# Optimization experiments

Measured on AMD Instinct MI355X. Metric: run time of the kernel, lower is better.

Reference implementation:

```python
import jax, jax.numpy as jnp
import numpy as np

B, S, H = 4, 1024, 896
NH, HD = 16, 56          # num_heads, head_dim (NH*HD == H)
SD = 896                 # ssm_state_dim
EPS = 1e-5


def _ln(v, g, b):
    m = jnp.mean(v, axis=-1, keepdims=True)
    var = jnp.var(v, axis=-1, keepdims=True)
    return (v - m) * jax.lax.rsqrt(var + EPS) * g + b


def setup_inputs() -> dict:
    key = jax.random.key(0)
    ks = jax.random.split(key, 24)
    n = lambda k, sh, s=0.02: jax.random.normal(k, sh, dtype=jnp.float32) * s
    return {
        "x": jax.random.normal(ks[0], (B, S, H), dtype=jnp.float32),
        # SSM params
        "A": n(ks[1], (SD, SD), 0.05),
        "Bm": n(ks[2], (SD, H), 0.05),
        "Cm": n(ks[3], (H, SD), 0.05),
        "ssm_in_w": n(ks[4], (H, H)), "ssm_in_b": n(ks[5], (H,)),
        "ssm_out_w": n(ks[6], (H, H)), "ssm_out_b": n(ks[7], (H,)),
        # MHA params (torch in_proj packs q,k,v)
        "qkv_w": n(ks[8], (3 * H, H)), "qkv_b": n(ks[9], (3 * H,)),
        "attn_out_w": n(ks[10], (H, H)), "attn_out_b": n(ks[11], (H,)),
        "proj_w": n(ks[12], (H, H)), "proj_b": n(ks[13], (H,)),
        # LayerNorms
        "ln_ssm_g": jnp.ones((H,), jnp.float32), "ln_ssm_b": jnp.zeros((H,), jnp.float32),
        "ln_attn_g": jnp.ones((H,), jnp.float32), "ln_attn_b": jnp.zeros((H,), jnp.float32),
        # Mixer
        "fuse_w": n(ks[14], (H, 3 * H)), "fuse_b": n(ks[15], (H,)),
        "gate_w": n(ks[16], (2, H)), "gate_b": n(ks[17], (2,)),
    }


def reference(x, A, Bm, Cm, ssm_in_w, ssm_in_b, ssm_out_w, ssm_out_b,
              qkv_w, qkv_b, attn_out_w, attn_out_b, proj_w, proj_b,
              ln_ssm_g, ln_ssm_b, ln_attn_g, ln_attn_b,
              fuse_w, fuse_b, gate_w, gate_b):
    # ---- SSM head: h_t = tanh(h_{t-1} A^T + x_t B^T); y_t = h_t C^T ----
    xp = x @ ssm_in_w.T + ssm_in_b                     # (B,S,H)
    xB = xp @ Bm.T                                     # precompute input drive (B,S,SD)

    def step(h, xb_t):
        h = jnp.tanh(h @ A.T + xb_t)
        return h, h

    h0 = jnp.zeros((B, SD), x.dtype)
    _, hs = jax.lax.scan(step, h0, jnp.swapaxes(xB, 0, 1))   # hs: (S,B,SD)
    ys = jnp.swapaxes(hs, 0, 1) @ Cm.T                 # (B,S,H)
    ssm_out = ys @ ssm_out_w.T + ssm_out_b

    # ---- Attention head: standard non-causal MHA + extra projection ----
    qkv = x @ qkv_w.T + qkv_b                          # (B,S,3H)
    q, k, v = jnp.split(qkv, 3, axis=-1)
    q = q.reshape(B, S, NH, HD)
    k = k.reshape(B, S, NH, HD)
    v = v.reshape(B, S, NH, HD)
    scores = jnp.einsum("bqhd,bkhd->bhqk", q, k) / np.sqrt(HD).astype(np.float32)
    attn = jax.nn.softmax(scores, axis=-1)
    ctx = jnp.einsum("bhqk,bkhd->bqhd", attn, v).reshape(B, S, H)
    attn_out = (ctx @ attn_out_w.T + attn_out_b) @ proj_w.T + proj_b

    # ---- Gate norms ----
    ssm_g = _ln(ssm_out, ln_ssm_g, ln_ssm_b)
    attn_g = _ln(attn_out, ln_attn_g, ln_attn_b)

    # ---- Mixing network (memory_state=None -> zero padding) ----
    combined = jnp.concatenate([ssm_g, attn_g, jnp.zeros_like(ssm_g)], axis=-1)
    fused = combined @ fuse_w.T + fuse_b
    gates = jax.nn.softmax(fused @ gate_w.T + gate_b, axis=-1)   # (B,S,2)
    out = gates[..., 0:1] * ssm_g + gates[..., 1:2] * attn_g
    return out  # dropout is identity in eval mode
```

## Files before the change

kernel.cpp:

```cpp
#include <hip/hip_runtime.h>
#include <hip/hip_bf16.h>

typedef __bf16 bf16;
typedef __bf16 bf16x8 __attribute__((ext_vector_type(8)));
typedef __bf16 bf16x4 __attribute__((ext_vector_type(4)));
typedef float  f32x4  __attribute__((ext_vector_type(4)));

__global__ __launch_bounds__(256, 2)
void gemm128_kernel(const float* __restrict__ A, const float* __restrict__ B,
                    const float* __restrict__ bias, float* __restrict__ C,
                    int M, int N, int K, int lda, int ldb, int ldc)
{
    __shared__ bf16 As[128][72];
    __shared__ bf16 Bs[128][72];
    const int tid = threadIdx.x;
    const long bm = (long)blockIdx.y * 128;
    const long bn = (long)blockIdx.x * 128;
    const int w  = tid >> 6;
    const int l  = tid & 63;
    const int wm = (w >> 1) * 64, wn = (w & 1) * 64;
    const int lr = l & 15, lk = (l >> 4) * 8;

    const int srow = tid >> 1;
    const int scol = (tid & 1) * 32;
    const float* Ap = A + (bm + srow) * (long)lda + scol;
    const float* Bp = B + (bn + srow) * (long)ldb + scol;

    f32x4 acc[4][4];
    #pragma unroll
    for (int i = 0; i < 4; ++i)
        #pragma unroll
        for (int j = 0; j < 4; ++j)
            acc[i][j] = f32x4{0.f, 0.f, 0.f, 0.f};

    for (int kt = 0; kt < K; kt += 64) {
        #pragma unroll
        for (int i = 0; i < 32; i += 4) {
            float4 av = *reinterpret_cast<const float4*>(Ap + kt + i);
            float4 bv = *reinterpret_cast<const float4*>(Bp + kt + i);
            bf16x4 ac; ac[0] = (bf16)av.x; ac[1] = (bf16)av.y; ac[2] = (bf16)av.z; ac[3] = (bf16)av.w;
            bf16x4 bc; bc[0] = (bf16)bv.x; bc[1] = (bf16)bv.y; bc[2] = (bf16)bv.z; bc[3] = (bf16)bv.w;
            *reinterpret_cast<bf16x4*>(&As[srow][scol + i]) = ac;
            *reinterpret_cast<bf16x4*>(&Bs[srow][scol + i]) = bc;
        }
        __syncthreads();
        #pragma unroll
        for (int kk = 0; kk < 64; kk += 32) {
            bf16x8 a[4], b[4];
            #pragma unroll
            for (int i = 0; i < 4; ++i) {
                a[i] = *reinterpret_cast<const bf16x8*>(&As[wm + i * 16 + lr][kk + lk]);
                b[i] = *reinterpret_cast<const bf16x8*>(&Bs[wn + i * 16 + lr][kk + lk]);
            }
            #pragma unroll
            for (int i = 0; i < 4; ++i)
                #pragma unroll
                for (int j = 0; j < 4; ++j)
                    acc[i][j] = __builtin_amdgcn_mfma_f32_16x16x32_bf16(a[i], b[j], acc[i][j], 0, 0, 0);
        }
        __syncthreads();
    }
    const int crow = wm + (l >> 4) * 4;
    const int ccol = wn + (l & 15);
    #pragma unroll
    for (int i = 0; i < 4; ++i)
        #pragma unroll
        for (int j = 0; j < 4; ++j) {
            long col = bn + ccol + j * 16;
            float bv = bias ? bias[col] : 0.0f;
            #pragma unroll
            for (int r = 0; r < 4; ++r) {
                long row = bm + crow + i * 16 + r;
                C[row * (long)ldc + col] = acc[i][j][r] + bv;
            }
        }
}

#define SENT64 0xFFFFFFFFFFFFFFFFull
#define NBLK_SCAN 56

__device__ __forceinline__ float lo32f(unsigned long long v) {
    return __builtin_bit_cast(float, (unsigned int)v);
}
__device__ __forceinline__ float hi32f(unsigned long long v) {
    return __builtin_bit_cast(float, (unsigned int)(v >> 32));
}

__device__ __forceinline__ void scan_body(const float* __restrict__ Amat,
                                          const float* __restrict__ xB,
                                          float* __restrict__ hs,
                                          unsigned long long* __restrict__ Y,
                                          float* hS)
{
    __builtin_amdgcn_s_setprio(3);
    const int tid = threadIdx.x;
    const int bi  = blockIdx.x;
    const int kq  = tid & 31;
    const int rg  = tid >> 5;
    const int row = bi * 16 + rg;

    float4 areg[7];
    {
        const float4* Ap = reinterpret_cast<const float4*>(Amat + (long)row * 896 + kq * 28);
        #pragma unroll
        for (int j = 0; j < 7; ++j) areg[j] = Ap[j];
    }

    const int d0 = tid;
    const int d1 = tid + 512;
    const bool two = (tid < 384);

    for (int t = 1; t <= 1024; ++t) {
        const long so = (long)(t - 1) * 896 + row;
        float xb0 = 0, xb1 = 0, xb2 = 0, xb3 = 0;
        if (kq == 0) {
            xb0 = xB[so];
            xb1 = xB[so +  917504];
            xb2 = xB[so + 1835008];
            xb3 = xB[so + 2752512];
        }

        if (t == 1) {
            #pragma unroll
            for (int j = 0; j < 7; ++j) hS[tid + j * 512] = 0.0f;
        } else {
            const unsigned long long* Yp = Y + (long)(t - 2) * 1792;
            unsigned long long va, vb, vc = 0, vd = 0;
            for (;;) {
                va = __hip_atomic_load(&Yp[2 * d0],     __ATOMIC_RELAXED, __HIP_MEMORY_SCOPE_AGENT);
                vb = __hip_atomic_load(&Yp[2 * d0 + 1], __ATOMIC_RELAXED, __HIP_MEMORY_SCOPE_AGENT);
                bool ok = (va != SENT64) & (vb != SENT64);
                if (two) {
                    vc = __hip_atomic_load(&Yp[2 * d1],     __ATOMIC_RELAXED, __HIP_MEMORY_SCOPE_AGENT);
                    vd = __hip_atomic_load(&Yp[2 * d1 + 1], __ATOMIC_RELAXED, __HIP_MEMORY_SCOPE_AGENT);
                    ok &= (vc != SENT64) & (vd != SENT64);
                }
                if (ok) break;
                __builtin_amdgcn_s_sleep(1);
            }
            hS[       d0] = lo32f(va);
            hS[ 896 + d0] = hi32f(va);
            hS[1792 + d0] = lo32f(vb);
            hS[2688 + d0] = hi32f(vb);
            if (two) {
                hS[       d1] = lo32f(vc);
                hS[ 896 + d1] = hi32f(vc);
                hS[1792 + d1] = lo32f(vd);
                hS[2688 + d1] = hi32f(vd);
            }
        }
        __syncthreads();

        const float4* h0p = reinterpret_cast<const float4*>(hS +    0 + kq * 28);
        const float4* h1p = reinterpret_cast<const float4*>(hS +  896 + kq * 28);
        const float4* h2p = reinterpret_cast<const float4*>(hS + 1792 + kq * 28);
        const float4* h3p = reinterpret_cast<const float4*>(hS + 2688 + kq * 28);
        float a0 = 0, a1 = 0, a2 = 0, a3 = 0;
        #pragma unroll
        for (int j = 0; j < 7; ++j) {
            float4 a = areg[j];
            float4 v0 = h0p[j]; a0 += a.x*v0.x + a.y*v0.y + a.z*v0.z + a.w*v0.w;
            float4 v1 = h1p[j]; a1 += a.x*v1.x + a.y*v1.y + a.z*v1.z + a.w*v1.w;
            float4 v2 = h2p[j]; a2 += a.x*v2.x + a.y*v2.y + a.z*v2.z + a.w*v2.w;
            float4 v3 = h3p[j]; a3 += a.x*v3.x + a.y*v3.y + a.z*v3.z + a.w*v3.w;
        }
        a0 += __shfl_xor(a0, 16); a1 += __shfl_xor(a1, 16); a2 += __shfl_xor(a2, 16); a3 += __shfl_xor(a3, 16);
        a0 += __shfl_xor(a0,  8); a1 += __shfl_xor(a1,  8); a2 += __shfl_xor(a2,  8); a3 += __shfl_xor(a3,  8);
        a0 += __shfl_xor(a0,  4); a1 += __shfl_xor(a1,  4); a2 += __shfl_xor(a2,  4); a3 += __shfl_xor(a3,  4);
        a0 += __shfl_xor(a0,  2); a1 += __shfl_xor(a1,  2); a2 += __shfl_xor(a2,  2); a3 += __shfl_xor(a3,  2);
        a0 += __shfl_xor(a0,  1); a1 += __shfl_xor(a1,  1); a2 += __shfl_xor(a2,  1); a3 += __shfl_xor(a3,  1);

        if (kq == 0) {
            float z[4] = { a0 + xb0, a1 + xb1, a2 + xb2, a3 + xb3 };
            float hv[4];
            #pragma unroll
            for (int b = 0; b < 4; ++b) {
                float zz = fminf(fmaxf(z[b], -15.f), 15.f);
                float e  = __expf(2.f * zz);
                hv[b] = (e - 1.f) / (e + 1.f);
            }
            unsigned long long lo =
                (unsigned long long)__builtin_bit_cast(unsigned int, hv[0]) |
                ((unsigned long long)__builtin_bit_cast(unsigned int, hv[1]) << 32);
            unsigned long long hi =
                (unsigned long long)__builtin_bit_cast(unsigned int, hv[2]) |
                ((unsigned long long)__builtin_bit_cast(unsigned int, hv[3]) << 32);
            unsigned long long* yp = Y + (long)(t - 1) * 1792 + 2 * row;
            __hip_atomic_store(&yp[0], lo, __ATOMIC_RELAXED, __HIP_MEMORY_SCOPE_AGENT);
            __hip_atomic_store(&yp[1], hi, __ATOMIC_RELAXED, __HIP_MEMORY_SCOPE_AGENT);
            #pragma unroll
            for (int b = 0; b < 4; ++b)
                hs[(long)b * 917504 + so] = hv[b];
        }
        __syncthreads();
    }
}

__device__ __forceinline__ void attn_body(const float* __restrict__ qkv,
                                          float* __restrict__ ctx,
                                          float* ldsf, int bid2)
{
    float* qS = ldsf;
    float* pS = qS + 1792;
    float* rS = pS + 2112;
    float* lS = rS + 32;
    bf16*  kS = (bf16*)(lS + 32);
    bf16*  vS = kS + 3840;

    const int tid = threadIdx.x;
    const int qc = bid2 & 31;
    const int h  = (bid2 >> 5) & 15;
    const int b  = bid2 >> 9;
    const long base = (long)b * 1024 * 2688;
    const int q0 = qc * 32;
    const int hoff = h * 56;

    for (int idx = tid; idx < 1792; idx += 512) {
        int r = idx / 56, d = idx - r * 56;
        qS[idx] = qkv[base + (long)(q0 + r) * 2688 + hoff + d] * 0.13363062095621f;
    }

    const int w = tid >> 6, l = tid & 63;
    const int qrow = 4 * w;
    const int oq = tid >> 4, ods = tid & 15;
    float m0 = -3e38f, m1 = -3e38f, m2 = -3e38f, m3 = -3e38f;
    float s_l0 = 0, s_l1 = 0, s_l2 = 0, s_l3 = 0;
    float o0 = 0, o1 = 0, o2 = 0, o3 = 0;

    for (int kt = 0; kt < 16; ++kt) {
        __syncthreads();
        for (int idx = tid; idx < 3584; idx += 512) {
            int r = idx / 56, d = idx - r * 56;
            long g = base + (long)(kt * 64 + r) * 2688 + hoff + d;
            kS[r * 60 + d] = (bf16)qkv[g + 896];
            vS[r * 60 + d] = (bf16)qkv[g + 1792];
        }
        __syncthreads();

        float s0 = 0, s1 = 0, s2 = 0, s3 = 0;
        const float* qp = qS + qrow * 56;
        const bf16* kp = kS + l * 60;
        #pragma unroll 8
        for (int d = 0; d < 56; ++d) {
            float kv = (float)kp[d];
            s0 += qp[d] * kv; s1 += qp[d + 56] * kv;
            s2 += qp[d + 112] * kv; s3 += qp[d + 168] * kv;
        }
        float x0 = s0, x1 = s1, x2 = s2, x3 = s3;
        #pragma unroll
        for (int off = 32; off >= 1; off >>= 1) {
            x0 = fmaxf(x0, __shfl_xor(x0, off));
            x1 = fmaxf(x1, __shfl_xor(x1, off));
            x2 = fmaxf(x2, __shfl_xor(x2, off));
            x3 = fmaxf(x3, __shfl_xor(x3, off));
        }
        float nm0 = fmaxf(m0, x0), nm1 = fmaxf(m1, x1);
        float nm2 = fmaxf(m2, x2), nm3 = fmaxf(m3, x3);
        float p0 = __expf(s0 - nm0), p1 = __expf(s1 - nm1);
        float p2 = __expf(s2 - nm2), p3 = __expf(s3 - nm3);
        float sc0 = __expf(m0 - nm0), sc1 = __expf(m1 - nm1);
        float sc2 = __expf(m2 - nm2), sc3 = __expf(m3 - nm3);
        float t0 = p0, t1 = p1, t2 = p2, t3 = p3;
        #pragma unroll
        for (int off = 32; off >= 1; off >>= 1) {
            t0 += __shfl_xor(t0, off); t1 += __shfl_xor(t1, off);
            t2 += __shfl_xor(t2, off); t3 += __shfl_xor(t3, off);
        }
        s_l0 = s_l0 * sc0 + t0; s_l1 = s_l1 * sc1 + t1;
        s_l2 = s_l2 * sc2 + t2; s_l3 = s_l3 * sc3 + t3;
        m0 = nm0; m1 = nm1; m2 = nm2; m3 = nm3;
        pS[(qrow + 0) * 66 + l] = p0; pS[(qrow + 1) * 66 + l] = p1;
        pS[(qrow + 2) * 66 + l] = p2; pS[(qrow + 3) * 66 + l] = p3;
        if (l == 0) { rS[qrow] = sc0; rS[qrow+1] = sc1; rS[qrow+2] = sc2; rS[qrow+3] = sc3; }
        __syncthreads();

        float rf = rS[oq];
        o0 *= rf; o1 *= rf; o2 *= rf; o3 *= rf;
        const float* pp = pS + oq * 66;
        #pragma unroll 4
        for (int kk = 0; kk < 64; ++kk) {
            float p = pp[kk];
            const bf16* vp = vS + kk * 60 + ods;
            o0 += p * (float)vp[0];
            o1 += p * (float)vp[16];
            o2 += p * (float)vp[32];
            if (ods < 8) o3 += p * (float)vp[48];
        }
    }
    __syncthreads();
    if (l == 0) {
        lS[qrow]     = 1.f / s_l0; lS[qrow + 1] = 1.f / s_l1;
        lS[qrow + 2] = 1.f / s_l2; lS[qrow + 3] = 1.f / s_l3;
    }
    __syncthreads();
    float inv = lS[oq];
    float* cp = ctx + ((long)b * 1024 + q0 + oq) * 896 + hoff + ods;
    cp[0]  = o0 * inv;
    cp[16] = o1 * inv;
    cp[32] = o2 * inv;
    if (ods < 8) cp[48] = o3 * inv;
}

__global__ __launch_bounds__(512)
void scan_attn_kernel(const float* __restrict__ Amat, const float* __restrict__ xB,
                      float* __restrict__ hs, unsigned long long* __restrict__ Y,
                      const float* __restrict__ qkv, float* __restrict__ ctx)
{
    __shared__ float ldsf[7872];
    if (blockIdx.x < NBLK_SCAN)
        scan_body(Amat, xB, hs, Y, ldsf);
    else
        attn_body(qkv, ctx, ldsf, blockIdx.x - NBLK_SCAN);
}

__global__ __launch_bounds__(256)
void ln2_kernel(const float* __restrict__ s_in, const float* __restrict__ a_in,
                const float* __restrict__ gs, const float* __restrict__ bs,
                const float* __restrict__ ga, const float* __restrict__ ba,
                float* __restrict__ comb)
{
    const int wv = threadIdx.x >> 6, ln = threadIdx.x & 63;
    const long row = (long)blockIdx.x * 4 + wv;
    const bool is_a = (blockIdx.y != 0);
    const float* src = (is_a ? a_in : s_in) + row * 896;
    float v[14]; float sum = 0, sq = 0;
    #pragma unroll
    for (int j = 0; j < 14; ++j) { v[j] = src[ln + j * 64]; sum += v[j]; sq += v[j] * v[j]; }
    #pragma unroll
    for (int off = 32; off >= 1; off >>= 1) { sum += __shfl_xor(sum, off); sq += __shfl_xor(sq, off); }
    const float mean = sum * (1.0f / 896.0f);
    const float var  = sq * (1.0f / 896.0f) - mean * mean;
    const float inv  = rsqrtf(var + 1e-5f);
    const float* g  = is_a ? ga : gs;
    const float* bb = is_a ? ba : bs;
    float* dst = comb + row * 1792 + (is_a ? 896 : 0);
    #pragma unroll
    for (int j = 0; j < 14; ++j) {
        int i = ln + j * 64;
        dst[i] = (v[j] - mean) * inv * g[i] + bb[i];
    }
}

__global__ __launch_bounds__(256)
void gate_mix_kernel(const float* __restrict__ fused, const float* __restrict__ gw,
                     const float* __restrict__ gb, const float* __restrict__ comb,
                     float* __restrict__ out)
{
    const int tid = threadIdx.x;
    const int seg = tid & 15;
    const long row = (long)blockIdx.x * 16 + (tid >> 4);
    const float* fr = fused + row * 896;
    float d0 = 0, d1 = 0;
    for (int i = seg; i < 896; i += 16) {
        float f = fr[i];
        d0 += f * gw[i];
        d1 += f * gw[896 + i];
    }
    #pragma unroll
    for (int off = 8; off >= 1; off >>= 1) { d0 += __shfl_xor(d0, off); d1 += __shfl_xor(d1, off); }
    float l0 = d0 + gb[0], l1 = d1 + gb[1];
    float m = fmaxf(l0, l1);
    float e0 = __expf(l0 - m), e1 = __expf(l1 - m);
    float inv = 1.0f / (e0 + e1);
    float g0 = e0 * inv, g1 = e1 * inv;
    const float* cr = comb + row * 1792;
    float* orow = out + row * 896;
    for (int i = seg; i < 896; i += 16)
        orow[i] = g0 * cr[i] + g1 * cr[896 + i];
}

extern "C" void kernel_launch(void* const* d_in, const int* in_sizes, int n_in,
                              void* d_out, int out_size, void* d_ws, size_t ws_size,
                              hipStream_t stream)
{
    (void)in_sizes; (void)n_in; (void)out_size; (void)ws_size;
    const float* x         = (const float*)d_in[0];
    const float* Amat      = (const float*)d_in[1];
    const float* Bm        = (const float*)d_in[2];
    const float* Cm        = (const float*)d_in[3];
    const float* ssm_in_w  = (const float*)d_in[4];
    const float* ssm_in_b  = (const float*)d_in[5];
    const float* ssm_out_w = (const float*)d_in[6];
    const float* ssm_out_b = (const float*)d_in[7];
    const float* qkv_w     = (const float*)d_in[8];
    const float* qkv_b     = (const float*)d_in[9];
    const float* attn_w    = (const float*)d_in[10];
    const float* attn_b    = (const float*)d_in[11];
    const float* proj_w    = (const float*)d_in[12];
    const float* proj_b    = (const float*)d_in[13];
    const float* ln_sg     = (const float*)d_in[14];
    const float* ln_sb     = (const float*)d_in[15];
    const float* ln_ag     = (const float*)d_in[16];
    const float* ln_ab     = (const float*)d_in[17];
    const float* fuse_w    = (const float*)d_in[18];
    const float* fuse_b    = (const float*)d_in[19];
    const float* gate_w    = (const float*)d_in[20];
    const float* gate_b    = (const float*)d_in[21];

    float* ws = (float*)d_ws;
    const long S0 = 0;
    const long S1 = 3670016;
    const long S2 = 7340032;
    const long S3 = 18350080;
    const long S4 = 22020096;
    const long S5 = 25690112;
    const long S6 = 33030144;

    dim3 g128(7, 32), gqkv(21, 32);

    gemm128_kernel<<<g128, 256, 0, stream>>>(x, ssm_in_w, ssm_in_b, ws + S0, 4096, 896, 896, 896, 896, 896);
    gemm128_kernel<<<g128, 256, 0, stream>>>(ws + S0, Bm, nullptr, ws + S1, 4096, 896, 896, 896, 896, 896);
    hipMemsetAsync(ws + S0, 0xFF, 3670016 * sizeof(float), stream);
    gemm128_kernel<<<gqkv, 256, 0, stream>>>(x, qkv_w, qkv_b, ws + S2, 4096, 2688, 896, 896, 896, 2688);
    scan_attn_kernel<<<NBLK_SCAN + 2048, 512, 0, stream>>>(
        Amat, ws + S1, ws + S3, (unsigned long long*)(ws + S0), ws + S2, ws + S6);
    gemm128_kernel<<<g128, 256, 0, stream>>>(ws + S3, Cm, nullptr, ws + S0, 4096, 896, 896, 896, 896, 896);
    gemm128_kernel<<<g128, 256, 0, stream>>>(ws + S0, ssm_out_w, ssm_out_b, ws + S4, 4096, 896, 896, 896, 896, 896);
    gemm128_kernel<<<g128, 256, 0, stream>>>(ws + S6, attn_w, attn_b, ws + S1, 4096, 896, 896, 896, 896, 896);
    gemm128_kernel<<<g128, 256, 0, stream>>>(ws + S1, proj_w, proj_b, ws + S3, 4096, 896, 896, 896, 896, 896);
    ln2_kernel<<<dim3(1024, 2), 256, 0, stream>>>(ws + S4, ws + S3, ln_sg, ln_sb, ln_ag, ln_ab, ws + S5);
    gemm128_kernel<<<g128, 256, 0, stream>>>(ws + S5, fuse_w, fuse_b, ws + S4, 4096, 896, 1792, 1792, 2688, 896);
    gate_mix_kernel<<<256, 256, 0, stream>>>(ws + S4, gate_w, gate_b, ws + S5, (float*)d_out);
}
```

Baseline: 3.225 ms.

## Convert operands to bf16 upfront and stream GEMM tiles via global_load_lds

Adds a batched fp32-to-bf16 conversion kernel for x and the weights. The GEMM now takes bf16 operands and loads tiles straight into LDS with global_load_lds instead of converting in registers. Intermediate activations (hs, ctx, xp, ys, comb) are written as bf16 so the following GEMMs read half the bytes, and the scan's barriers become a bare s_barrier after an lgkmcnt wait. In exchange it adds conversion launches, drops the LDS row padding (which may cause bank conflicts), and takes on a more complex workspace aliasing plan.

```diff
diff --git a/kernel.cpp b/kernel.cpp
--- a/kernel.cpp
+++ b/kernel.cpp
@@ -6,25 +6,54 @@
 typedef __bf16 bf16x4 __attribute__((ext_vector_type(4)));
 typedef float  f32x4  __attribute__((ext_vector_type(4)));
 
+#define AS1 __attribute__((address_space(1)))
+#define AS3 __attribute__((address_space(3)))
+
+struct CvtArgs {
+    const float* src[5];
+    bf16* dst[5];
+    int rows[5], cols[5], src_ld[5];
+};
+
+__global__ __launch_bounds__(256)
+void cvt_kernel(CvtArgs a)
+{
+    const int t = blockIdx.y;
+    const float* s = a.src[t];
+    bf16* d = a.dst[t];
+    const int cols = a.cols[t];
+    const long total = (long)a.rows[t] * cols;
+    const int ld = a.src_ld[t];
+    for (long i = ((long)blockIdx.x * 256 + threadIdx.x) * 4; i < total;
+         i += (long)gridDim.x * 1024) {
+        long r = i / cols, c = i - r * cols;
+        float4 v = *reinterpret_cast<const float4*>(s + r * ld + c);
+        bf16x4 o; o[0] = (bf16)v.x; o[1] = (bf16)v.y; o[2] = (bf16)v.z; o[3] = (bf16)v.w;
+        *reinterpret_cast<bf16x4*>(d + i) = o;
+    }
+}
+
 __global__ __launch_bounds__(256, 2)
-void gemm128_kernel(const float* __restrict__ A, const float* __restrict__ B,
-                    const float* __restrict__ bias, float* __restrict__ C,
-                    int M, int N, int K, int lda, int ldb, int ldc)
-{
-    __shared__ bf16 As[128][72];
-    __shared__ bf16 Bs[128][72];
+void gemm_bf16_kernel(const bf16* __restrict__ A, const bf16* __restrict__ B,
+                      const float* __restrict__ bias,
+                      float* __restrict__ Cf, bf16* __restrict__ Cb,
+                      int M, int N, int K)
+{
+    __shared__ bf16 As[128 * 64];
+    __shared__ bf16 Bs[128 * 64];
     const int tid = threadIdx.x;
     const long bm = (long)blockIdx.y * 128;
     const long bn = (long)blockIdx.x * 128;
-    const int w  = tid >> 6;
-    const int l  = tid & 63;
+    const int w  = tid >> 6, l = tid & 63;
     const int wm = (w >> 1) * 64, wn = (w & 1) * 64;
     const int lr = l & 15, lk = (l >> 4) * 8;
 
-    const int srow = tid >> 1;
-    const int scol = (tid & 1) * 32;
-    const float* Ap = A + (bm + srow) * (long)lda + scol;
-    const float* Bp = B + (bn + srow) * (long)ldb + scol;
+    const int srow = tid >> 3;
+    const int scol = (tid & 7) * 8;
+    const bf16* Ag = A + (bm + srow) * (long)K + scol;
+    const bf16* Bg = B + (bn + srow) * (long)K + scol;
+    bf16* AsW = As + srow * 64 + scol;
+    bf16* BsW = Bs + srow * 64 + scol;
 
     f32x4 acc[4][4];
     #pragma unroll
@@ -35,13 +64,13 @@
 
     for (int kt = 0; kt < K; kt += 64) {
         #pragma unroll
-        for (int i = 0; i < 32; i += 4) {
-            float4 av = *reinterpret_cast<const float4*>(Ap + kt + i);
-            float4 bv = *reinterpret_cast<const float4*>(Bp + kt + i);
-            bf16x4 ac; ac[0] = (bf16)av.x; ac[1] = (bf16)av.y; ac[2] = (bf16)av.z; ac[3] = (bf16)av.w;
-            bf16x4 bc; bc[0] = (bf16)bv.x; bc[1] = (bf16)bv.y; bc[2] = (bf16)bv.z; bc[3] = (bf16)bv.w;
-            *reinterpret_cast<bf16x4*>(&As[srow][scol + i]) = ac;
-            *reinterpret_cast<bf16x4*>(&Bs[srow][scol + i]) = bc;
+        for (int i = 0; i < 4; ++i) {
+            __builtin_amdgcn_global_load_lds(
+                (const AS1 void*)(Ag + (long)i * 32 * K + kt),
+                (AS3 void*)(AsW + i * 2048), 16, 0, 0);
+            __builtin_amdgcn_global_load_lds(
+                (const AS1 void*)(Bg + (long)i * 32 * K + kt),
+                (AS3 void*)(BsW + i * 2048), 16, 0, 0);
         }
         __syncthreads();
         #pragma unroll
@@ -49,8 +78,8 @@
             bf16x8 a[4], b[4];
             #pragma unroll
             for (int i = 0; i < 4; ++i) {
-                a[i] = *reinterpret_cast<const bf16x8*>(&As[wm + i * 16 + lr][kk + lk]);
-                b[i] = *reinterpret_cast<const bf16x8*>(&Bs[wn + i * 16 + lr][kk + lk]);
+                a[i] = *reinterpret_cast<const bf16x8*>(&As[(wm + i * 16 + lr) * 64 + kk + lk]);
+                b[i] = *reinterpret_cast<const bf16x8*>(&Bs[(wn + i * 16 + lr) * 64 + kk + lk]);
             }
             #pragma unroll
             for (int i = 0; i < 4; ++i)
@@ -71,7 +100,9 @@
             #pragma unroll
             for (int r = 0; r < 4; ++r) {
                 long row = bm + crow + i * 16 + r;
-                C[row * (long)ldc + col] = acc[i][j][r] + bv;
+                float v = acc[i][j][r] + bv;
+                if (Cf) Cf[row * (long)N + col] = v;
+                if (Cb) Cb[row * (long)N + col] = (bf16)v;
             }
         }
 }
@@ -79,6 +110,11 @@
 #define SENT64 0xFFFFFFFFFFFFFFFFull
 #define NBLK_SCAN 56
 
+__device__ __forceinline__ void bar_lgkm() {
+    asm volatile("s_waitcnt lgkmcnt(0)" ::: "memory");
+    __builtin_amdgcn_s_barrier();
+}
+
 __device__ __forceinline__ float lo32f(unsigned long long v) {
     return __builtin_bit_cast(float, (unsigned int)v);
 }
@@ -88,7 +124,7 @@
 
 __device__ __forceinline__ void scan_body(const float* __restrict__ Amat,
                                           const float* __restrict__ xB,
-                                          float* __restrict__ hs,
+                                          bf16* __restrict__ hs16,
                                           unsigned long long* __restrict__ Y,
                                           float* hS)
 {
@@ -149,7 +185,7 @@
                 hS[2688 + d1] = hi32f(vd);
             }
         }
-        __syncthreads();
+        bar_lgkm();
 
         const float4* h0p = reinterpret_cast<const float4*>(hS +    0 + kq * 28);
         const float4* h1p = reinterpret_cast<const float4*>(hS +  896 + kq * 28);
@@ -190,14 +226,14 @@
             __hip_atomic_store(&yp[1], hi, __ATOMIC_RELAXED, __HIP_MEMORY_SCOPE_AGENT);
             #pragma unroll
             for (int b = 0; b < 4; ++b)
-                hs[(long)b * 917504 + so] = hv[b];
-        }
-        __syncthreads();
+                hs16[(long)b * 917504 + so] = (bf16)hv[b];
+        }
+        bar_lgkm();
     }
 }
 
 __device__ __forceinline__ void attn_body(const float* __restrict__ qkv,
-                                          float* __restrict__ ctx,
+                                          bf16* __restrict__ ctx16,
                                           float* ldsf, int bid2)
 {
     float* qS = ldsf;
@@ -294,30 +330,30 @@
     }
     __syncthreads();
     float inv = lS[oq];
-    float* cp = ctx + ((long)b * 1024 + q0 + oq) * 896 + hoff + ods;
-    cp[0]  = o0 * inv;
-    cp[16] = o1 * inv;
-    cp[32] = o2 * inv;
-    if (ods < 8) cp[48] = o3 * inv;
+    bf16* cp = ctx16 + ((long)b * 1024 + q0 + oq) * 896 + hoff + ods;
+    cp[0]  = (bf16)(o0 * inv);
+    cp[16] = (bf16)(o1 * inv);
+    cp[32] = (bf16)(o2 * inv);
+    if (ods < 8) cp[48] = (bf16)(o3 * inv);
 }
 
 __global__ __launch_bounds__(512)
 void scan_attn_kernel(const float* __restrict__ Amat, const float* __restrict__ xB,
-                      float* __restrict__ hs, unsigned long long* __restrict__ Y,
-                      const float* __restrict__ qkv, float* __restrict__ ctx)
+                      bf16* __restrict__ hs16, unsigned long long* __restrict__ Y,
+                      const float* __restrict__ qkv, bf16* __restrict__ ctx16)
 {
     __shared__ float ldsf[7872];
     if (blockIdx.x < NBLK_SCAN)
-        scan_body(Amat, xB, hs, Y, ldsf);
+        scan_body(Amat, xB, hs16, Y, ldsf);
     else
-        attn_body(qkv, ctx, ldsf, blockIdx.x - NBLK_SCAN);
+        attn_body(qkv, ctx16, ldsf, blockIdx.x - NBLK_SCAN);
 }
 
 __global__ __launch_bounds__(256)
 void ln2_kernel(const float* __restrict__ s_in, const float* __restrict__ a_in,
                 const float* __restrict__ gs, const float* __restrict__ bs,
                 const float* __restrict__ ga, const float* __restrict__ ba,
-                float* __restrict__ comb)
+                float* __restrict__ comb, bf16* __restrict__ comb16)
 {
     const int wv = threadIdx.x >> 6, ln = threadIdx.x & 63;
     const long row = (long)blockIdx.x * 4 + wv;
@@ -333,11 +369,14 @@
     const float inv  = rsqrtf(var + 1e-5f);
     const float* g  = is_a ? ga : gs;
     const float* bb = is_a ? ba : bs;
-    float* dst = comb + row * 1792 + (is_a ? 896 : 0);
+    float* dst   = comb   + row * 1792 + (is_a ? 896 : 0);
+    bf16*  dst16 = comb16 + row * 1792 + (is_a ? 896 : 0);
     #pragma unroll
     for (int j = 0; j < 14; ++j) {
         int i = ln + j * 64;
-        dst[i] = (v[j] - mean) * inv * g[i] + bb[i];
+        float o = (v[j] - mean) * inv * g[i] + bb[i];
+        dst[i] = o;
+        dst16[i] = (bf16)o;
     }
 }
 
@@ -397,28 +436,59 @@
     const float* gate_w    = (const float*)d_in[20];
     const float* gate_b    = (const float*)d_in[21];
 
-    float* ws = (float*)d_ws;
-    const long S0 = 0;
-    const long S1 = 3670016;
-    const long S2 = 7340032;
-    const long S3 = 18350080;
-    const long S4 = 22020096;
-    const long S5 = 25690112;
-    const long S6 = 33030144;
-
-    dim3 g128(7, 32), gqkv(21, 32);
-
-    gemm128_kernel<<<g128, 256, 0, stream>>>(x, ssm_in_w, ssm_in_b, ws + S0, 4096, 896, 896, 896, 896, 896);
-    gemm128_kernel<<<g128, 256, 0, stream>>>(ws + S0, Bm, nullptr, ws + S1, 4096, 896, 896, 896, 896, 896);
-    hipMemsetAsync(ws + S0, 0xFF, 3670016 * sizeof(float), stream);
-    gemm128_kernel<<<gqkv, 256, 0, stream>>>(x, qkv_w, qkv_b, ws + S2, 4096, 2688, 896, 896, 896, 2688);
-    scan_attn_kernel<<<NBLK_SCAN + 2048, 512, 0, stream>>>(
-        Amat, ws + S1, ws + S3, (unsigned long long*)(ws + S0), ws + S2, ws + S6);
-    gemm128_kernel<<<g128, 256, 0, stream>>>(ws + S3, Cm, nullptr, ws + S0, 4096, 896, 896, 896, 896, 896);
-    gemm128_kernel<<<g128, 256, 0, stream>>>(ws + S0, ssm_out_w, ssm_out_b, ws + S4, 4096, 896, 896, 896, 896, 896);
-    gemm128_kernel<<<g128, 256, 0, stream>>>(ws + S6, attn_w, attn_b, ws + S1, 4096, 896, 896, 896, 896, 896);
-    gemm128_kernel<<<g128, 256, 0, stream>>>(ws + S1, proj_w, proj_b, ws + S3, 4096, 896, 896, 896, 896, 896);
-    ln2_kernel<<<dim3(1024, 2), 256, 0, stream>>>(ws + S4, ws + S3, ln_sg, ln_sb, ln_ag, ln_ab, ws + S5);
-    gemm128_kernel<<<g128, 256, 0, stream>>>(ws + S5, fuse_w, fuse_b, ws + S4, 4096, 896, 1792, 1792, 2688, 896);
-    gate_mix_kernel<<<256, 256, 0, stream>>>(ws + S4, gate_w, gate_b, ws + S5, (float*)d_out);
-}
+    float* wsf = (float*)d_ws;
+    char*  wsb = (char*)d_ws;
+
+    unsigned long long* Y = (unsigned long long*)wsb;
+    float* xB       = wsf + 3670016;
+    float* qkv      = wsf + 7340032;
+    float* attn_out = wsf + 18350080;
+    float* ssm_out  = wsf + 22020096;
+    float* combf    = wsf + 25690112;
+    bf16* comb16 = (bf16*)wsb;
+    bf16* ssm_in_w16 = (bf16*)(wsb + 73400320);
+    bf16* Bm16       = (bf16*)(wsb + 75005952);
+    bf16* qkv_w16    = (bf16*)(wsb + 76611584);
+    bf16* hs16   = (bf16*)(wsb + 73400320);
+    bf16* ys16   = (bf16*)(wsb + 80740352);
+    bf16* Cm16        = (bf16*)(wsb + 14680064);
+    bf16* ssm_out_w16 = (bf16*)(wsb + 16285696);
+    bf16* attn_w16    = (bf16*)(wsb + 17891328);
+    bf16* proj_w16    = (bf16*)(wsb + 19496960);
+    bf16* fuse_w16    = (bf16*)(wsb + 21102592);
+    bf16* ctx16  = (bf16*)(wsb + 102760448);
+    bf16* t116   = (bf16*)(wsb + 110100480);
+    bf16* x16    = (bf16*)(wsb + 132120576);
+    bf16* xp16   = (bf16*)(wsb + 139460608);
+
+    hipMemsetAsync(Y, 0xFF, 14680064, stream);
+
+    CvtArgs c1{};
+    c1.src[0] = x;        c1.dst[0] = x16;        c1.rows[0] = 1;    c1.cols[0] = 3670016; c1.src_ld[0] = 3670016;
+    c1.src[1] = ssm_in_w; c1.dst[1] = ssm_in_w16; c1.rows[1] = 1;    c1.cols[1] = 802816;  c1.src_ld[1] = 802816;
+    c1.src[2] = Bm;       c1.dst[2] = Bm16;       c1.rows[2] = 1;    c1.cols[2] = 802816;  c1.src_ld[2] = 802816;
+    c1.src[3] = qkv_w;    c1.dst[3] = qkv_w16;    c1.rows[3] = 1;    c1.cols[3] = 2408448; c1.src_ld[3] = 2408448;
+    c1.src[4] = x;        c1.dst[4] = x16;        c1.rows[4] = 1;    c1.cols[4] = 0;       c1.src_ld[4] = 4;
+    cvt_kernel<<<dim3(64, 4), 256, 0, stream>>>(c1);
+
+    gemm_bf16_kernel<<<dim3(7, 32),  256, 0, stream>>>(x16,  ssm_in_w16, ssm_in_b, nullptr, xp16, 4096, 896, 896);
+    gemm_bf16_kernel<<<dim3(7, 32),  256, 0, stream>>>(xp16, Bm16,       nullptr,  xB, nullptr,  4096, 896, 896);
+    gemm_bf16_kernel<<<dim3(21, 32), 256, 0, stream>>>(x16,  qkv_w16,    qkv_b,    qkv, nullptr, 4096, 2688, 896);
+    scan_attn_kernel<<<NBLK_SCAN + 2048, 512, 0, stream>>>(Amat, xB, hs16, Y, qkv, ctx16);
+
+    CvtArgs c2{};
+    c2.src[0] = Cm;        c2.dst[0] = Cm16;        c2.rows[0] = 1;   c2.cols[0] = 802816; c2.src_ld[0] = 802816;
+    c2.src[1] = ssm_out_w; c2.dst[1] = ssm_out_w16; c2.rows[1] = 1;   c2.cols[1] = 802816; c2.src_ld[1] = 802816;
+    c2.src[2] = attn_w;    c2.dst[2] = attn_w16;    c2.rows[2] = 1;   c2.cols[2] = 802816; c2.src_ld[2] = 802816;
+    c2.src[3] = proj_w;    c2.dst[3] = proj_w16;    c2.rows[3] = 1;   c2.cols[3] = 802816; c2.src_ld[3] = 802816;
+    c2.src[4] = fuse_w;    c2.dst[4] = fuse_w16;    c2.rows[4] = 896; c2.cols[4] = 1792;   c2.src_ld[4] = 2688;
+    cvt_kernel<<<dim3(64, 5), 256, 0, stream>>>(c2);
+
+    gemm_bf16_kernel<<<dim3(7, 32), 256, 0, stream>>>(hs16, Cm16,        nullptr,   nullptr, ys16, 4096, 896, 896);
+    gemm_bf16_kernel<<<dim3(7, 32), 256, 0, stream>>>(ys16, ssm_out_w16, ssm_out_b, ssm_out, nullptr, 4096, 896, 896);
+    gemm_bf16_kernel<<<dim3(7, 32), 256, 0, stream>>>(ctx16, attn_w16, attn_b, nullptr, t116, 4096, 896, 896);
+    gemm_bf16_kernel<<<dim3(7, 32), 256, 0, stream>>>(t116,  proj_w16, proj_b, attn_out, nullptr, 4096, 896, 896);
+    ln2_kernel<<<dim3(1024, 2), 256, 0, stream>>>(ssm_out, attn_out, ln_sg, ln_sb, ln_ag, ln_ab, combf, comb16);
+    gemm_bf16_kernel<<<dim3(7, 32), 256, 0, stream>>>(comb16, fuse_w16, fuse_b, ssm_out, nullptr, 4096, 896, 1792);
+    gate_mix_kernel<<<256, 256, 0, stream>>>(ssm_out, gate_w, gate_b, combf, (float*)d_out);
+}
```

New measurement: 3.118 ms. 3.3% less time.
